# Kernel tuning notes

Measured on AMD Instinct MI355X. Metric: run time of the kernel, lower is better.

Reference implementation:

```python
import jax, jax.numpy as jnp
import numpy as np

ES = 256
NUM_SPECIES, NUM_ABILITIES, NUM_ITEMS, NUM_MOVES = 1026, 300, 500, 920
NUM_ITEM_EFFECTS, NUM_GENDERS, NUM_STATUS, NUM_VOLATILE_STATUS = 16, 3, 8, 105
B, N, F = 8192, 12, 42
# feature layout (flat int32 vector per entity)
(SPECIES, ABILITY, ITEM, ITEM_EFFECT, GENDER, STATUS, BEING_CALLED_BACK, TRAPPED,
 NEWLY_SWITCHED, TOXIC_TURNS, SLEEP_TURNS, FAINTED, ACTIVE, SIDE, LEVEL, HP, MAXHP) = range(17)
BOOST0, VOL0, MOVEID0, MOVEPP0 = 17, 24, 33, 37  # 7 boosts, 9 volatile words, 4 moves, 4 pp

DENSE_DIMS = [("hp", 10), ("level", 7), ("active", 2), ("onehot", 32), ("boosts", 7),
              ("volatiles", NUM_VOLATILE_STATUS), ("item", ES + NUM_ITEM_EFFECTS),
              ("side", 2), ("moves", ES + 6)]

def _bits(x, world_dim):
    # binary-scale embedding: bit decomposition of an int feature
    nb = (world_dim - 1).bit_length()
    mask = jnp.asarray(1 << np.arange(nb), dtype=jnp.int32)
    return ((x[..., None] & mask) != 0).astype(jnp.float32)

def setup_inputs() -> dict:
    key = jax.random.key(0)
    ks = jax.random.split(key, 32)
    s = 0.02
    inp = {"entities": jax.random.randint(ks[0], (B, N, F), 0, 2, dtype=jnp.int32)}
    inp["embed_species"] = jax.random.normal(ks[1], (NUM_SPECIES, ES), jnp.float32) * s
    inp["embed_ability"] = jax.random.normal(ks[2], (NUM_ABILITIES, ES), jnp.float32) * s
    inp["embed_item"] = jax.random.normal(ks[3], (NUM_ITEMS, ES), jnp.float32) * s
    inp["embed_moves"] = jax.random.normal(ks[4], (NUM_MOVES, ES), jnp.float32) * s
    for i, (name, din) in enumerate(DENSE_DIMS):
        inp[f"{name}_W"] = jax.random.normal(ks[5 + i], (din, ES), jnp.float32) * s
        inp[f"{name}_b"] = jnp.zeros((ES,), jnp.float32)
    return inp

def _forward(entities, embed_species, embed_ability, embed_item, embed_moves,
             hp_W, hp_b, level_W, level_b, active_W, active_b, onehot_W, onehot_b,
             boosts_W, boosts_b, volatiles_W, volatiles_b, item_W, item_b,
             side_W, side_b, moves_W, moves_b):
    e = entities
    oh = jax.nn.one_hot
    dense = lambda x, W, b: x @ W + b
    hp = e[..., HP].astype(jnp.float32)
    maxhp = jnp.clip(e[..., MAXHP], 1).astype(jnp.float32)
    hp_ratio = jnp.clip(hp / maxhp, 0.0, 1.0)                      # (B,N)
    hp_token = jnp.floor(1023.0 * hp_ratio).astype(jnp.int32)
    boolean_code = jnp.concatenate([
        hp_ratio[..., None], oh(e[..., GENDER], NUM_GENDERS), oh(e[..., STATUS], NUM_STATUS),
        oh(e[..., BEING_CALLED_BACK], 2), oh(e[..., TRAPPED], 2), oh(e[..., NEWLY_SWITCHED], 2),
        oh(e[..., TOXIC_TURNS], 8), oh(e[..., SLEEP_TURNS], 4), oh(e[..., FAINTED], 2)], axis=-1)  # (B,N,32)
    item_onehot = jnp.concatenate([embed_item[e[..., ITEM]], oh(e[..., ITEM_EFFECT], NUM_ITEM_EFFECTS)], axis=-1)
    boosts = e[..., BOOST0:VOL0].astype(jnp.float32) / 2.0          # (B,N,7)
    vol = e[..., VOL0:VOL0 + 9]
    vbits = (vol[..., None] & jnp.arange(16)) > 0                   # (B,N,9,16)
    vol_oh = vbits.reshape(*vol.shape[:-1], 144)[..., :NUM_VOLATILE_STATUS].astype(jnp.float32)
    moveset = jnp.concatenate([embed_moves[e[..., MOVEID0:MOVEPP0]],
                               _bits(e[..., MOVEPP0:MOVEPP0 + 4], 64)], axis=-1)  # (B,N,4,262)
    moves_out = jnp.einsum('bnmf,fd->bnd', moveset, moves_W) + 4.0 * moves_b      # sum of 4 Dense outputs
    emb = (dense(_bits(hp_token, 1024), hp_W, hp_b)
           + dense(_bits(e[..., LEVEL], 101), level_W, level_b)
           + dense(oh(e[..., ACTIVE], 2), active_W, active_b)
           + dense(boolean_code, onehot_W, onehot_b)
           + dense(boosts, boosts_W, boosts_b)
           + dense(vol_oh, volatiles_W, volatiles_b)
           + embed_species[e[..., SPECIES]]
           + embed_ability[e[..., ABILITY]]
           + dense(item_onehot, item_W, item_b)
           + dense(oh(e[..., SIDE], 2), side_W, side_b)
           + moves_out)
    return emb

def reference(entities, embed_species, embed_ability, embed_item, embed_moves,
              hp_W, hp_b, level_W, level_b, active_W, active_b, onehot_W, onehot_b,
              boosts_W, boosts_b, volatiles_W, volatiles_b, item_W, item_b,
              side_W, side_b, moves_W, moves_b):
    return _forward(entities, embed_species, embed_ability, embed_item, embed_moves,
                    hp_W, hp_b, level_W, level_b, active_W, active_b, onehot_W, onehot_b,
                    boosts_W, boosts_b, volatiles_W, volatiles_b, item_W, item_b,
                    side_W, side_b, moves_W, moves_b)
```

## Files before the change

### kernel.cpp

```cpp
#include <hip/hip_runtime.h>

#define ES 256
#define NFEAT 42
#define NENT (8192 * 12)

#define F_SPECIES 0
#define F_ABILITY 1
#define F_ITEM 2
#define F_ITEM_EFFECT 3
#define F_GENDER 4
#define F_STATUS 5
#define F_BCB 6
#define F_TRAPPED 7
#define F_NEWSW 8
#define F_TOXIC 9
#define F_SLEEP 10
#define F_FAINTED 11
#define F_ACTIVE 12
#define F_SIDE 13
#define F_LEVEL 14
#define F_HP 15
#define F_MAXHP 16
#define F_BOOST0 17
#define F_VOL0 24
#define F_MOVEID0 33
#define F_MOVEPP0 37

#define OFF_HP     0
#define OFF_LV     (OFF_HP + 1024*ES)
#define OFF_PP     (OFF_LV + 128*ES)
#define OFF_VP     (OFF_PP + 64*ES)
#define OFF_CA     (OFF_VP + 784*ES)
#define OFF_CB     (OFF_CA + 768*ES)
#define OFF_EITEM  (OFF_CB + 1024*ES)
#define OFF_EMOVES (OFF_EITEM + 500*ES)

typedef float vf4 __attribute__((ext_vector_type(4)));

__device__ __forceinline__ float4 ld4(const float* p) {
    return *reinterpret_cast<const float4*>(p);
}
__device__ __forceinline__ void st4(float* p, const float4 v) {
    *reinterpret_cast<float4*>(p) = v;
}
__device__ __forceinline__ void st4_nt(float* p, const float4 v) {
    vf4 t = {v.x, v.y, v.z, v.w};
    __builtin_nontemporal_store(t, reinterpret_cast<vf4*>(p));
}
__device__ __forceinline__ void add4(float4& a, const float4 b) {
    a.x += b.x; a.y += b.y; a.z += b.z; a.w += b.w;
}
__device__ __forceinline__ float4 sum4(const float4 a, const float4 b) {
    return make_float4(a.x + b.x, a.y + b.y, a.z + b.z, a.w + b.w);
}
__device__ __forceinline__ void fma4(float4& a, float s, const float4 b) {
    a.x += s * b.x; a.y += s * b.y; a.z += s * b.z; a.w += s * b.w;
}
__device__ __forceinline__ int sclamp(int x, int lo, int hi) {
    return x < lo ? lo : (x > hi ? hi : x);
}

#define TB_HP0 0
#define TB_LV0 256
#define TB_PP0 288
#define TB_VP0 304
#define TB_CA0 500
#define TB_CB0 692
#define TB_EI0 948
#define TB_EM0 1073
#define TB_TOT 1303

__global__ __launch_bounds__(256) void k_tables(
    const float* __restrict__ item_e, const float* __restrict__ moves_e,
    const float* __restrict__ hp_W, const float* __restrict__ level_W,
    const float* __restrict__ moves_W, const float* __restrict__ vol_W,
    const float* __restrict__ item_W, const float* __restrict__ onehot_W,
    const float* __restrict__ active_W, const float* __restrict__ side_W,
    const float* __restrict__ hp_b, const float* __restrict__ level_b,
    const float* __restrict__ active_b, const float* __restrict__ onehot_b,
    const float* __restrict__ boosts_b, const float* __restrict__ vol_b,
    const float* __restrict__ item_b, const float* __restrict__ side_b,
    const float* __restrict__ moves_b,
    float* __restrict__ ws) {
    __shared__ float4 se4[4][64];
    const int bid = blockIdx.x, tid = threadIdx.x;
    const int rl = tid >> 6, lane = tid & 63, d0 = lane * 4;
    float4 acc = make_float4(0.f, 0.f, 0.f, 0.f);

    if (bid < TB_LV0) {
        int v = (bid - TB_HP0) * 4 + rl;
        for (int b = 0; b < 10; ++b)
            if ((v >> b) & 1) add4(acc, ld4(hp_W + b * ES + d0));
        st4(ws + OFF_HP + v * ES + d0, acc);
    } else if (bid < TB_PP0) {
        int v = (bid - TB_LV0) * 4 + rl;
        for (int b = 0; b < 7; ++b)
            if ((v >> b) & 1) add4(acc, ld4(level_W + b * ES + d0));
        st4(ws + OFF_LV + v * ES + d0, acc);
    } else if (bid < TB_VP0) {
        int v = (bid - TB_PP0) * 4 + rl;
        for (int b = 0; b < 6; ++b)
            if ((v >> b) & 1) add4(acc, ld4(moves_W + (256 + b) * ES + d0));
        st4(ws + OFF_PP + v * ES + d0, acc);
    } else if (bid < TB_CA0) {
        int v = (bid - TB_VP0) * 4 + rl;
        if (v < 768) {
            int t = v >> 8, pair = v & 255, a = pair >> 4, b = pair & 15;
            for (int j = 0; j < 16; ++j) {
                if (a & j) add4(acc, ld4(vol_W + (32 * t + j) * ES + d0));
                if (b & j) add4(acc, ld4(vol_W + (32 * t + 16 + j) * ES + d0));
            }
        } else {
            int a = v - 768;
            for (int j = 0; j < 9; ++j)
                if (a & j) add4(acc, ld4(vol_W + (96 + j) * ES + d0));
        }
        st4(ws + OFF_VP + v * ES + d0, acc);
    } else if (bid < TB_CB0) {
        int idx = (bid - TB_CA0) * 4 + rl;
        int fa = idx & 1, ns = (idx >> 1) & 1, tr = (idx >> 2) & 1, bcb = (idx >> 3) & 1;
        int rest = idx >> 4, g = rest % 3, e = rest / 3;
        acc = sum4(sum4(ld4(item_W + (256 + e) * ES + d0), ld4(onehot_W + (1 + g) * ES + d0)),
                   sum4(ld4(onehot_W + (12 + bcb) * ES + d0), ld4(onehot_W + (14 + tr) * ES + d0)));
        add4(acc, sum4(ld4(onehot_W + (16 + ns) * ES + d0), ld4(onehot_W + (30 + fa) * ES + d0)));
        st4(ws + OFF_CA + idx * ES + d0, acc);
    } else if (bid < TB_EI0) {
        int idx = (bid - TB_CB0) * 4 + rl;
        int sd = idx & 1, act = (idx >> 1) & 1, sl = (idx >> 2) & 3,
            tox = (idx >> 4) & 7, st = idx >> 7;
        acc = sum4(sum4(ld4(hp_b + d0), ld4(level_b + d0)),
                   sum4(ld4(active_b + d0), ld4(onehot_b + d0)));
        add4(acc, sum4(ld4(boosts_b + d0), ld4(vol_b + d0)));
        add4(acc, sum4(ld4(item_b + d0), ld4(side_b + d0)));
        fma4(acc, 4.0f, ld4(moves_b + d0));
        add4(acc, sum4(ld4(onehot_W + (4 + st) * ES + d0), ld4(onehot_W + (18 + tox) * ES + d0)));
        add4(acc, sum4(ld4(onehot_W + (26 + sl) * ES + d0),
                       sum4(ld4(active_W + act * ES + d0), ld4(side_W + sd * ES + d0))));
        st4(ws + OFF_CB + idx * ES + d0, acc);
    } else {
        const float* E; const float* W; float* o; int r0;
        if (bid < TB_EM0) { E = item_e;  W = item_W;  o = ws + OFF_EITEM;  r0 = (bid - TB_EI0) * 4; }
        else              { E = moves_e; W = moves_W; o = ws + OFF_EMOVES; r0 = (bid - TB_EM0) * 4; }
        se4[tid >> 6][tid & 63] = ld4(E + r0 * ES + tid * 4);
        __syncthreads();
#pragma unroll 4
        for (int k0 = 0; k0 < 64; ++k0) {
            float4 e4 = se4[rl][k0];
            fma4(acc, e4.x, ld4(W + (4 * k0 + 0) * ES + d0));
            fma4(acc, e4.y, ld4(W + (4 * k0 + 1) * ES + d0));
            fma4(acc, e4.z, ld4(W + (4 * k0 + 2) * ES + d0));
            fma4(acc, e4.w, ld4(W + (4 * k0 + 3) * ES + d0));
        }
        st4(o + (r0 + rl) * ES + d0, acc);
    }
}


__global__ __launch_bounds__(256) void k_main(
    const int* __restrict__ ent,
    const float* __restrict__ spW, const float* __restrict__ abW,
    const float* __restrict__ onehotW, const float* __restrict__ boostsW,
    const float* __restrict__ ws,
    float* __restrict__ out) {
    const int lane = threadIdx.x & 63;
    const int went = __builtin_amdgcn_readfirstlane((blockIdx.x * 256 + threadIdx.x) >> 6);
    const int d0 = lane * 4;

    int fv = ent[went * NFEAT + (lane < NFEAT ? lane : 0)];
#define RL(i) __builtin_amdgcn_readlane(fv, (i))

    const float* Hp     = ws + OFF_HP;
    const float* Lv     = ws + OFF_LV;
    const float* Pp     = ws + OFF_PP;
    const float* VP     = ws + OFF_VP;
    const float* CA     = ws + OFF_CA;
    const float* CB     = ws + OFF_CB;
    const float* Eitem  = ws + OFF_EITEM;
    const float* Emoves = ws + OFF_EMOVES;

    const int iB = ((((RL(F_STATUS) & 7) * 8 + (RL(F_TOXIC) & 7)) * 4 + (RL(F_SLEEP) & 3)) * 2 +
                    (RL(F_ACTIVE) & 1)) * 2 + (RL(F_SIDE) & 1);
    const int iA = (((((RL(F_ITEM_EFFECT) & 15) * 3 + sclamp(RL(F_GENDER), 0, 2)) * 2 +
                      (RL(F_BCB) & 1)) * 2 + (RL(F_TRAPPED) & 1)) * 2 +
                    (RL(F_NEWSW) & 1)) * 2 + (RL(F_FAINTED) & 1);
    const int iSP = sclamp(RL(F_SPECIES), 0, 1025);
    const int iAB = sclamp(RL(F_ABILITY), 0, 299);
    const int iIT = sclamp(RL(F_ITEM), 0, 499);
    const float hp = (float)RL(F_HP);
    int mh = RL(F_MAXHP); if (mh < 1) mh = 1;
    const float ratio = fminf(fmaxf(hp / (float)mh, 0.f), 1.f);
    const int tok = __builtin_amdgcn_readfirstlane((int)floorf(1023.f * ratio));
    const int iLV = RL(F_LEVEL) & 127;
    const int b0 = RL(F_BOOST0 + 0), b1 = RL(F_BOOST0 + 1), b2 = RL(F_BOOST0 + 2),
              b3 = RL(F_BOOST0 + 3), b4 = RL(F_BOOST0 + 4), b5 = RL(F_BOOST0 + 5),
              b6 = RL(F_BOOST0 + 6);
    const int vp0 = ((RL(F_VOL0 + 0) & 15) << 4) | (RL(F_VOL0 + 1) & 15);
    const int vp1 = ((RL(F_VOL0 + 2) & 15) << 4) | (RL(F_VOL0 + 3) & 15);
    const int vp2 = ((RL(F_VOL0 + 4) & 15) << 4) | (RL(F_VOL0 + 5) & 15);
    const int v6  = RL(F_VOL0 + 6) & 15;
    const int m0 = sclamp(RL(F_MOVEID0 + 0), 0, 919), m1 = sclamp(RL(F_MOVEID0 + 1), 0, 919),
              m2 = sclamp(RL(F_MOVEID0 + 2), 0, 919), m3 = sclamp(RL(F_MOVEID0 + 3), 0, 919);
    const int p0 = RL(F_MOVEPP0 + 0) & 63, p1 = RL(F_MOVEPP0 + 1) & 63,
              p2 = RL(F_MOVEPP0 + 2) & 63, p3 = RL(F_MOVEPP0 + 3) & 63;
#undef RL

    const float4 xCB  = ld4(CB + iB * ES + d0);
    const float4 xCA  = ld4(CA + iA * ES + d0);
    const float4 xSP  = ld4(spW + iSP * ES + d0);
    const float4 xAB  = ld4(abW + iAB * ES + d0);
    const float4 xIT  = ld4(Eitem + iIT * ES + d0);
    const float4 xHP  = ld4(Hp + tok * ES + d0);
    const float4 xOH  = ld4(onehotW + d0);
    const float4 xLV  = ld4(Lv + iLV * ES + d0);
    const float4 xV0  = ld4(VP + (0 * 256 + vp0) * ES + d0);
    const float4 xV1  = ld4(VP + (1 * 256 + vp1) * ES + d0);
    const float4 xV2  = ld4(VP + (2 * 256 + vp2) * ES + d0);
    const float4 xV6  = ld4(VP + (768 + v6) * ES + d0);
    const float4 xE0  = ld4(Emoves + m0 * ES + d0);
    const float4 xE1  = ld4(Emoves + m1 * ES + d0);
    const float4 xE2  = ld4(Emoves + m2 * ES + d0);
    const float4 xE3  = ld4(Emoves + m3 * ES + d0);
    const float4 xP0  = ld4(Pp + p0 * ES + d0);
    const float4 xP1  = ld4(Pp + p1 * ES + d0);
    const float4 xP2  = ld4(Pp + p2 * ES + d0);
    const float4 xP3  = ld4(Pp + p3 * ES + d0);
    const float4 xB0  = ld4(boostsW + 0 * ES + d0);
    const float4 xB1  = ld4(boostsW + 1 * ES + d0);
    const float4 xB2  = ld4(boostsW + 2 * ES + d0);
    const float4 xB3  = ld4(boostsW + 3 * ES + d0);
    const float4 xB4  = ld4(boostsW + 4 * ES + d0);
    const float4 xB5  = ld4(boostsW + 5 * ES + d0);
    const float4 xB6  = ld4(boostsW + 6 * ES + d0);

    float4 s0 = sum4(sum4(xCB, xCA), sum4(xSP, xAB));
    float4 s1 = sum4(sum4(xIT, xHP), sum4(xLV, xV6));
    float4 s2 = sum4(sum4(xV0, xV1), sum4(xV2, xE0));
    float4 s3 = sum4(sum4(xE1, xE2), sum4(xE3, xP0));
    float4 s4 = sum4(sum4(xP1, xP2), xP3);
    float4 acc = sum4(sum4(s0, s1), sum4(s2, s3));
    add4(acc, s4);
    fma4(acc, ratio, xOH);
    fma4(acc, 0.5f * (float)b0, xB0);
    fma4(acc, 0.5f * (float)b1, xB1);
    fma4(acc, 0.5f * (float)b2, xB2);
    fma4(acc, 0.5f * (float)b3, xB3);
    fma4(acc, 0.5f * (float)b4, xB4);
    fma4(acc, 0.5f * (float)b5, xB5);
    fma4(acc, 0.5f * (float)b6, xB6);

    st4_nt(out + went * ES + d0, acc);
}


extern "C" void kernel_launch(void* const* d_in, const int* in_sizes, int n_in,
                              void* d_out, int out_size, void* d_ws, size_t ws_size,
                              hipStream_t stream) {
    const int*   entities = (const int*)  d_in[0];
    const float* sp       = (const float*)d_in[1];
    const float* ab       = (const float*)d_in[2];
    const float* item_e   = (const float*)d_in[3];
    const float* moves_e  = (const float*)d_in[4];
    const float* hp_W     = (const float*)d_in[5];
    const float* hp_b     = (const float*)d_in[6];
    const float* level_W  = (const float*)d_in[7];
    const float* level_b  = (const float*)d_in[8];
    const float* active_W = (const float*)d_in[9];
    const float* active_b = (const float*)d_in[10];
    const float* onehot_W = (const float*)d_in[11];
    const float* onehot_b = (const float*)d_in[12];
    const float* boosts_W = (const float*)d_in[13];
    const float* boosts_b = (const float*)d_in[14];
    const float* vol_W    = (const float*)d_in[15];
    const float* vol_b    = (const float*)d_in[16];
    const float* item_W   = (const float*)d_in[17];
    const float* item_b   = (const float*)d_in[18];
    const float* side_W   = (const float*)d_in[19];
    const float* side_b   = (const float*)d_in[20];
    const float* moves_W  = (const float*)d_in[21];
    const float* moves_b  = (const float*)d_in[22];

    float* ws  = (float*)d_ws;
    float* out = (float*)d_out;

    k_tables<<<TB_TOT, 256, 0, stream>>>(item_e, moves_e, hp_W, level_W, moves_W, vol_W,
                                         item_W, onehot_W, active_W, side_W,
                                         hp_b, level_b, active_b, onehot_b, boosts_b,
                                         vol_b, item_b, side_b, moves_b, ws);

    k_main<<<NENT / 4, 256, 0, stream>>>(entities, sp, ab, onehot_W, boosts_W, ws, out);
}
```

Baseline: 251.3 us.

## Store precomputed lookup tables in fp16 and stage boost/onehot rows in LDS

All precomputed workspace tables are now written in half precision, and the species and ability embeddings are converted into fp16 copies by the table kernel. The main kernel gathers 8-byte fp16 chunks instead of 16-byte fp32 chunks, halving gather traffic and the cache footprint of the tables. The main kernel also stages the boost and onehot weight rows in shared memory once per block and loads entity features with a nontemporal load. The cost is fp16 rounding of every table term, which may push the output past tolerance, plus extra table-build blocks.

```diff
diff --git a/kernel.cpp b/kernel.cpp
--- a/kernel.cpp
+++ b/kernel.cpp
@@ -1,4 +1,5 @@
 #include <hip/hip_runtime.h>
+#include <hip/hip_fp16.h>
 
 #define ES 256
 #define NFEAT 42
@@ -32,8 +33,11 @@
 #define OFF_VP     (OFF_PP + 64*ES)
 #define OFF_CA     (OFF_VP + 784*ES)
 #define OFF_CB     (OFF_CA + 768*ES)
-#define OFF_EITEM  (OFF_CB + 1024*ES)
-#define OFF_EMOVES (OFF_EITEM + 500*ES)
+#define OFF_EI     (OFF_CB + 1024*ES)
+#define OFF_EM     (OFF_EI + 500*ES)
+#define OFF_SP     (OFF_EM + 920*ES)
+#define OFF_AB     (OFF_SP + 1026*ES)
+#define WS_HALVES  (OFF_AB + 300*ES)
 
 typedef float vf4 __attribute__((ext_vector_type(4)));
 
@@ -58,6 +62,21 @@
 }
 __device__ __forceinline__ int sclamp(int x, int lo, int hi) {
     return x < lo ? lo : (x > hi ? hi : x);
+}
+__device__ __forceinline__ void st4h(__half* p, const float4 v) {
+    __half2 a = __floats2half2_rn(v.x, v.y);
+    __half2 b = __floats2half2_rn(v.z, v.w);
+    uint2 u;
+    u.x = *reinterpret_cast<unsigned*>(&a);
+    u.y = *reinterpret_cast<unsigned*>(&b);
+    *reinterpret_cast<uint2*>(p) = u;
+}
+__device__ __forceinline__ float4 ldh4(const __half* p) {
+    uint2 u = *reinterpret_cast<const uint2*>(p);
+    __half2 a = *reinterpret_cast<__half2*>(&u.x);
+    __half2 b = *reinterpret_cast<__half2*>(&u.y);
+    float2 fa = __half22float2(a), fb = __half22float2(b);
+    return make_float4(fa.x, fa.y, fb.x, fb.y);
 }
 
 #define TB_HP0 0
@@ -68,9 +87,12 @@
 #define TB_CB0 692
 #define TB_EI0 948
 #define TB_EM0 1073
-#define TB_TOT 1303
+#define TB_SP0 1303
+#define TB_AB0 1560
+#define TB_TOT 1635
 
 __global__ __launch_bounds__(256) void k_tables(
+    const float* __restrict__ sp_e, const float* __restrict__ ab_e,
     const float* __restrict__ item_e, const float* __restrict__ moves_e,
     const float* __restrict__ hp_W, const float* __restrict__ level_W,
     const float* __restrict__ moves_W, const float* __restrict__ vol_W,
@@ -81,7 +103,7 @@
     const float* __restrict__ boosts_b, const float* __restrict__ vol_b,
     const float* __restrict__ item_b, const float* __restrict__ side_b,
     const float* __restrict__ moves_b,
-    float* __restrict__ ws) {
+    __half* __restrict__ wh) {
     __shared__ float4 se4[4][64];
     const int bid = blockIdx.x, tid = threadIdx.x;
     const int rl = tid >> 6, lane = tid & 63, d0 = lane * 4;
@@ -91,17 +113,17 @@
         int v = (bid - TB_HP0) * 4 + rl;
         for (int b = 0; b < 10; ++b)
             if ((v >> b) & 1) add4(acc, ld4(hp_W + b * ES + d0));
-        st4(ws + OFF_HP + v * ES + d0, acc);
+        st4h(wh + OFF_HP + v * ES + d0, acc);
     } else if (bid < TB_PP0) {
         int v = (bid - TB_LV0) * 4 + rl;
         for (int b = 0; b < 7; ++b)
             if ((v >> b) & 1) add4(acc, ld4(level_W + b * ES + d0));
-        st4(ws + OFF_LV + v * ES + d0, acc);
+        st4h(wh + OFF_LV + v * ES + d0, acc);
     } else if (bid < TB_VP0) {
         int v = (bid - TB_PP0) * 4 + rl;
         for (int b = 0; b < 6; ++b)
             if ((v >> b) & 1) add4(acc, ld4(moves_W + (256 + b) * ES + d0));
-        st4(ws + OFF_PP + v * ES + d0, acc);
+        st4h(wh + OFF_PP + v * ES + d0, acc);
     } else if (bid < TB_CA0) {
         int v = (bid - TB_VP0) * 4 + rl;
         if (v < 768) {
@@ -115,7 +137,7 @@
             for (int j = 0; j < 9; ++j)
                 if (a & j) add4(acc, ld4(vol_W + (96 + j) * ES + d0));
         }
-        st4(ws + OFF_VP + v * ES + d0, acc);
+        st4h(wh + OFF_VP + v * ES + d0, acc);
     } else if (bid < TB_CB0) {
         int idx = (bid - TB_CA0) * 4 + rl;
         int fa = idx & 1, ns = (idx >> 1) & 1, tr = (idx >> 2) & 1, bcb = (idx >> 3) & 1;
@@ -123,7 +145,7 @@
         acc = sum4(sum4(ld4(item_W + (256 + e) * ES + d0), ld4(onehot_W + (1 + g) * ES + d0)),
                    sum4(ld4(onehot_W + (12 + bcb) * ES + d0), ld4(onehot_W + (14 + tr) * ES + d0)));
         add4(acc, sum4(ld4(onehot_W + (16 + ns) * ES + d0), ld4(onehot_W + (30 + fa) * ES + d0)));
-        st4(ws + OFF_CA + idx * ES + d0, acc);
+        st4h(wh + OFF_CA + idx * ES + d0, acc);
     } else if (bid < TB_EI0) {
         int idx = (bid - TB_CB0) * 4 + rl;
         int sd = idx & 1, act = (idx >> 1) & 1, sl = (idx >> 2) & 3,
@@ -136,11 +158,11 @@
         add4(acc, sum4(ld4(onehot_W + (4 + st) * ES + d0), ld4(onehot_W + (18 + tox) * ES + d0)));
         add4(acc, sum4(ld4(onehot_W + (26 + sl) * ES + d0),
                        sum4(ld4(active_W + act * ES + d0), ld4(side_W + sd * ES + d0))));
-        st4(ws + OFF_CB + idx * ES + d0, acc);
-    } else {
-        const float* E; const float* W; float* o; int r0;
-        if (bid < TB_EM0) { E = item_e;  W = item_W;  o = ws + OFF_EITEM;  r0 = (bid - TB_EI0) * 4; }
-        else              { E = moves_e; W = moves_W; o = ws + OFF_EMOVES; r0 = (bid - TB_EM0) * 4; }
+        st4h(wh + OFF_CB + idx * ES + d0, acc);
+    } else if (bid < TB_SP0) {
+        const float* E; const float* W; __half* o; int r0;
+        if (bid < TB_EM0) { E = item_e;  W = item_W;  o = wh + OFF_EI; r0 = (bid - TB_EI0) * 4; }
+        else              { E = moves_e; W = moves_W; o = wh + OFF_EM; r0 = (bid - TB_EM0) * 4; }
         se4[tid >> 6][tid & 63] = ld4(E + r0 * ES + tid * 4);
         __syncthreads();
 #pragma unroll 4
@@ -151,32 +173,49 @@
             fma4(acc, e4.z, ld4(W + (4 * k0 + 2) * ES + d0));
             fma4(acc, e4.w, ld4(W + (4 * k0 + 3) * ES + d0));
         }
-        st4(o + (r0 + rl) * ES + d0, acc);
+        st4h(o + (r0 + rl) * ES + d0, acc);
+    } else if (bid < TB_AB0) {
+        int r = (bid - TB_SP0) * 4 + rl;
+        if (r < 1026) st4h(wh + OFF_SP + r * ES + d0, ld4(sp_e + r * ES + d0));
+    } else {
+        int r = (bid - TB_AB0) * 4 + rl;
+        st4h(wh + OFF_AB + r * ES + d0, ld4(ab_e + r * ES + d0));
     }
 }
 
 
 __global__ __launch_bounds__(256) void k_main(
     const int* __restrict__ ent,
-    const float* __restrict__ spW, const float* __restrict__ abW,
     const float* __restrict__ onehotW, const float* __restrict__ boostsW,
-    const float* __restrict__ ws,
+    const __half* __restrict__ wh,
     float* __restrict__ out) {
+    __shared__ float lds[8 * ES];
+    {
+        int t = threadIdx.x;
+        int row = t >> 5, col = (t & 31) * 8;
+        const float* src = (row < 7) ? (boostsW + row * ES + col) : (onehotW + col);
+        st4(&lds[row * ES + col], ld4(src));
+        st4(&lds[row * ES + col + 4], ld4(src + 4));
+    }
+    __syncthreads();
+
     const int lane = threadIdx.x & 63;
     const int went = __builtin_amdgcn_readfirstlane((blockIdx.x * 256 + threadIdx.x) >> 6);
     const int d0 = lane * 4;
 
-    int fv = ent[went * NFEAT + (lane < NFEAT ? lane : 0)];
+    int fv = __builtin_nontemporal_load(ent + went * NFEAT + (lane < NFEAT ? lane : 0));
 #define RL(i) __builtin_amdgcn_readlane(fv, (i))
 
-    const float* Hp     = ws + OFF_HP;
-    const float* Lv     = ws + OFF_LV;
-    const float* Pp     = ws + OFF_PP;
-    const float* VP     = ws + OFF_VP;
-    const float* CA     = ws + OFF_CA;
-    const float* CB     = ws + OFF_CB;
-    const float* Eitem  = ws + OFF_EITEM;
-    const float* Emoves = ws + OFF_EMOVES;
+    const __half* Hp = wh + OFF_HP;
+    const __half* Lv = wh + OFF_LV;
+    const __half* Pp = wh + OFF_PP;
+    const __half* VP = wh + OFF_VP;
+    const __half* CA = wh + OFF_CA;
+    const __half* CB = wh + OFF_CB;
+    const __half* EI = wh + OFF_EI;
+    const __half* EM = wh + OFF_EM;
+    const __half* SP = wh + OFF_SP;
+    const __half* AB = wh + OFF_AB;
 
     const int iB = ((((RL(F_STATUS) & 7) * 8 + (RL(F_TOXIC) & 7)) * 4 + (RL(F_SLEEP) & 3)) * 2 +
                     (RL(F_ACTIVE) & 1)) * 2 + (RL(F_SIDE) & 1);
@@ -204,49 +243,42 @@
               p2 = RL(F_MOVEPP0 + 2) & 63, p3 = RL(F_MOVEPP0 + 3) & 63;
 #undef RL
 
-    const float4 xCB  = ld4(CB + iB * ES + d0);
-    const float4 xCA  = ld4(CA + iA * ES + d0);
-    const float4 xSP  = ld4(spW + iSP * ES + d0);
-    const float4 xAB  = ld4(abW + iAB * ES + d0);
-    const float4 xIT  = ld4(Eitem + iIT * ES + d0);
-    const float4 xHP  = ld4(Hp + tok * ES + d0);
-    const float4 xOH  = ld4(onehotW + d0);
-    const float4 xLV  = ld4(Lv + iLV * ES + d0);
-    const float4 xV0  = ld4(VP + (0 * 256 + vp0) * ES + d0);
-    const float4 xV1  = ld4(VP + (1 * 256 + vp1) * ES + d0);
-    const float4 xV2  = ld4(VP + (2 * 256 + vp2) * ES + d0);
-    const float4 xV6  = ld4(VP + (768 + v6) * ES + d0);
-    const float4 xE0  = ld4(Emoves + m0 * ES + d0);
-    const float4 xE1  = ld4(Emoves + m1 * ES + d0);
-    const float4 xE2  = ld4(Emoves + m2 * ES + d0);
-    const float4 xE3  = ld4(Emoves + m3 * ES + d0);
-    const float4 xP0  = ld4(Pp + p0 * ES + d0);
-    const float4 xP1  = ld4(Pp + p1 * ES + d0);
-    const float4 xP2  = ld4(Pp + p2 * ES + d0);
-    const float4 xP3  = ld4(Pp + p3 * ES + d0);
-    const float4 xB0  = ld4(boostsW + 0 * ES + d0);
-    const float4 xB1  = ld4(boostsW + 1 * ES + d0);
-    const float4 xB2  = ld4(boostsW + 2 * ES + d0);
-    const float4 xB3  = ld4(boostsW + 3 * ES + d0);
-    const float4 xB4  = ld4(boostsW + 4 * ES + d0);
-    const float4 xB5  = ld4(boostsW + 5 * ES + d0);
-    const float4 xB6  = ld4(boostsW + 6 * ES + d0);
+    const float4 xCB = ldh4(CB + iB * ES + d0);
+    const float4 xCA = ldh4(CA + iA * ES + d0);
+    const float4 xSP = ldh4(SP + iSP * ES + d0);
+    const float4 xAB = ldh4(AB + iAB * ES + d0);
+    const float4 xIT = ldh4(EI + iIT * ES + d0);
+    const float4 xHP = ldh4(Hp + tok * ES + d0);
+    const float4 xLV = ldh4(Lv + iLV * ES + d0);
+    const float4 xV0 = ldh4(VP + (0 * 256 + vp0) * ES + d0);
+    const float4 xV1 = ldh4(VP + (1 * 256 + vp1) * ES + d0);
+    const float4 xV2 = ldh4(VP + (2 * 256 + vp2) * ES + d0);
+    const float4 xV6 = ldh4(VP + (768 + v6) * ES + d0);
+    const float4 xP0 = ldh4(Pp + p0 * ES + d0);
+    const float4 xP1 = ldh4(Pp + p1 * ES + d0);
+    const float4 xP2 = ldh4(Pp + p2 * ES + d0);
+    const float4 xP3 = ldh4(Pp + p3 * ES + d0);
+    const float4 xE0 = ldh4(EM + m0 * ES + d0);
+    const float4 xE1 = ldh4(EM + m1 * ES + d0);
+    const float4 xE2 = ldh4(EM + m2 * ES + d0);
+    const float4 xE3 = ldh4(EM + m3 * ES + d0);
 
     float4 s0 = sum4(sum4(xCB, xCA), sum4(xSP, xAB));
     float4 s1 = sum4(sum4(xIT, xHP), sum4(xLV, xV6));
-    float4 s2 = sum4(sum4(xV0, xV1), sum4(xV2, xE0));
-    float4 s3 = sum4(sum4(xE1, xE2), sum4(xE3, xP0));
+    float4 s2 = sum4(sum4(xV0, xV1), sum4(xV2, xP0));
+    float4 s3 = sum4(sum4(xE0, xE1), sum4(xE2, xE3));
     float4 s4 = sum4(sum4(xP1, xP2), xP3);
     float4 acc = sum4(sum4(s0, s1), sum4(s2, s3));
     add4(acc, s4);
-    fma4(acc, ratio, xOH);
-    fma4(acc, 0.5f * (float)b0, xB0);
-    fma4(acc, 0.5f * (float)b1, xB1);
-    fma4(acc, 0.5f * (float)b2, xB2);
-    fma4(acc, 0.5f * (float)b3, xB3);
-    fma4(acc, 0.5f * (float)b4, xB4);
-    fma4(acc, 0.5f * (float)b5, xB5);
-    fma4(acc, 0.5f * (float)b6, xB6);
+
+    fma4(acc, ratio, ld4(&lds[7 * ES + d0]));
+    fma4(acc, 0.5f * (float)b0, ld4(&lds[0 * ES + d0]));
+    fma4(acc, 0.5f * (float)b1, ld4(&lds[1 * ES + d0]));
+    fma4(acc, 0.5f * (float)b2, ld4(&lds[2 * ES + d0]));
+    fma4(acc, 0.5f * (float)b3, ld4(&lds[3 * ES + d0]));
+    fma4(acc, 0.5f * (float)b4, ld4(&lds[4 * ES + d0]));
+    fma4(acc, 0.5f * (float)b5, ld4(&lds[5 * ES + d0]));
+    fma4(acc, 0.5f * (float)b6, ld4(&lds[6 * ES + d0]));
 
     st4_nt(out + went * ES + d0, acc);
 }
@@ -279,13 +311,14 @@
     const float* moves_W  = (const float*)d_in[21];
     const float* moves_b  = (const float*)d_in[22];
 
-    float* ws  = (float*)d_ws;
-    float* out = (float*)d_out;
-
-    k_tables<<<TB_TOT, 256, 0, stream>>>(item_e, moves_e, hp_W, level_W, moves_W, vol_W,
-                                         item_W, onehot_W, active_W, side_W,
-                                         hp_b, level_b, active_b, onehot_b, boosts_b,
-                                         vol_b, item_b, side_b, moves_b, ws);
-
-    k_main<<<NENT / 4, 256, 0, stream>>>(entities, sp, ab, onehot_W, boosts_W, ws, out);
-}
+    __half* wh  = (__half*)d_ws;
+    float*  out = (float*)d_out;
+
+    k_tables<<<TB_TOT, 256, 0, stream>>>(
+        sp, ab, item_e, moves_e, hp_W, level_W, moves_W, vol_W,
+        item_W, onehot_W, active_W, side_W,
+        hp_b, level_b, active_b, onehot_b, boosts_b,
+        vol_b, item_b, side_b, moves_b, wh);
+
+    k_main<<<NENT / 4, 256, 0, stream>>>(entities, onehot_W, boosts_W, wh, out);
+}
```

Result: faster. 232.9 us (-7.3%).
